# Kernel optimization log

Hardware: AMD Instinct MI355X
Metric: run time of the kernel (lower is better)

## Reference

```python
import jax, jax.numpy as jnp
import numpy as np

D_MODEL = 1024
NUM_HEADS = 16
DEPTH = D_MODEL // NUM_HEADS
B, S = 2, 2048


def setup_inputs() -> dict:
    key = jax.random.key(0)
    ks = jax.random.split(key, 11)
    scale = 1.0 / np.sqrt(D_MODEL)
    inp = {
        "v": jax.random.normal(ks[0], (B, S, D_MODEL), dtype=jnp.float32),
        "k": jax.random.normal(ks[1], (B, S, D_MODEL), dtype=jnp.float32),
        "q": jax.random.normal(ks[2], (B, S, D_MODEL), dtype=jnp.float32),
        "wq": jax.random.normal(ks[3], (D_MODEL, D_MODEL), dtype=jnp.float32) * scale,
        "bq": jnp.zeros((D_MODEL,), dtype=jnp.float32),
        "wk": jax.random.normal(ks[4], (D_MODEL, D_MODEL), dtype=jnp.float32) * scale,
        "bk": jnp.zeros((D_MODEL,), dtype=jnp.float32),
        "wv": jax.random.normal(ks[5], (D_MODEL, D_MODEL), dtype=jnp.float32) * scale,
        "bv": jnp.zeros((D_MODEL,), dtype=jnp.float32),
        "wo": jax.random.normal(ks[6], (D_MODEL, D_MODEL), dtype=jnp.float32) * scale,
        "bo": jnp.zeros((D_MODEL,), dtype=jnp.float32),
    }
    return inp


def _split_heads(x):
    # (B, S, D) -> (B, H, S, depth)
    b, s, _ = x.shape
    return x.reshape(b, s, NUM_HEADS, DEPTH).transpose(0, 2, 1, 3)


def reference(v, k, q, wq, bq, wk, bk, wv, bv, wo, bo):
    qh = _split_heads(q @ wq + bq)  # (B,H,S,d)
    kh = _split_heads(k @ wk + bk)
    vh = _split_heads(v @ wv + bv)
    scores = jnp.einsum("bhqd,bhkd->bhqk", qh, kh) / jnp.sqrt(
        jnp.asarray(DEPTH, dtype=qh.dtype))
    attn = jax.nn.softmax(scores, axis=-1)
    out = jnp.einsum("bhqk,bhkd->bhqd", attn, vh)  # (B,H,S,d)
    out = out.transpose(0, 2, 1, 3).reshape(q.shape[0], -1, D_MODEL)
    return out @ wo + bo
```

## Files before the change

kernel.cpp:

```cpp
#include <hip/hip_runtime.h>
#include <hip/hip_bf16.h>

#define S_LEN 2048
#define DM 1024
#define NH 16
#define DH 64
#define MROWS 4096

typedef __hip_bfloat16 hbf;
typedef __attribute__((ext_vector_type(4))) float floatx4;
typedef __bf16 bf16x8 __attribute__((ext_vector_type(8)));

#define QSCALE 0.18033688f

#define GLOAD_LDS(g, l) __builtin_amdgcn_global_load_lds(                      \
    (const __attribute__((address_space(1))) void*)(g),                        \
    (__attribute__((address_space(3))) void*)(l), 16, 0, 0)


__global__ __launch_bounds__(256) void cvt3w(
    const float* __restrict__ q, const float* __restrict__ k, const float* __restrict__ v,
    hbf* __restrict__ Xqh, hbf* __restrict__ Xkh, hbf* __restrict__ Xvh,
    const float* __restrict__ wq, const float* __restrict__ wk,
    const float* __restrict__ wv, const float* __restrict__ wo,
    hbf* __restrict__ Wqh, hbf* __restrict__ Wkh,
    hbf* __restrict__ Wvh, hbf* __restrict__ Woh) {
  __shared__ float tile[64][65];
  const int t = threadIdx.x;
  if (blockIdx.y < 3) {
    const float* src; hbf* dst;
    switch (blockIdx.y) {
      case 0:  src = q; dst = Xqh; break;
      case 1:  src = k; dst = Xkh; break;
      default: src = v; dst = Xvh; break;
    }
    const int mt = blockIdx.x >> 4, kt = blockIdx.x & 15;
    const int s0 = mt * 64, k0 = kt * 64;
    const int lanep = t & 63, l15p = lanep & 15, quadp = lanep >> 4;
#pragma unroll
    for (int it = 0; it < 2; ++it) {
      int fl = (t >> 6) * 2 + it;
      int fm = fl >> 1, fk = fl & 1;
      const float* rp = &src[(size_t)(s0 + fm * 16 + l15p) * DM + k0 + fk * 32 + quadp * 8];
      const float4 v0 = *(const float4*)rp;
      const float4 v1 = *(const float4*)(rp + 4);
      union { hbf h[8]; uint4 u; } pk;
      pk.h[0] = __float2bfloat16(v0.x); pk.h[1] = __float2bfloat16(v0.y);
      pk.h[2] = __float2bfloat16(v0.z); pk.h[3] = __float2bfloat16(v0.w);
      pk.h[4] = __float2bfloat16(v1.x); pk.h[5] = __float2bfloat16(v1.y);
      pk.h[6] = __float2bfloat16(v1.z); pk.h[7] = __float2bfloat16(v1.w);
      size_t base = ((size_t)(mt * 4 + fm) * 32 + (kt * 2 + fk)) * 512 + lanep * 8;
      *(uint4*)&dst[base] = pk.u;
    }
    return;
  }
  const float* W; hbf* Wh;
  switch (blockIdx.x >> 8) {
    case 0:  W = wq; Wh = Wqh; break;
    case 1:  W = wk; Wh = Wkh; break;
    case 2:  W = wv; Wh = Wvh; break;
    default: W = wo; Wh = Woh; break;
  }
  const int t8 = blockIdx.x & 255;
  const int n0 = (t8 & 15) * 64, k0 = (t8 >> 4) * 64;
  const int c4 = (t & 15) * 4, r16 = t >> 4;
#pragma unroll
  for (int i = 0; i < 4; ++i) {
    int row = i * 16 + r16;
    const float4 vv = *(const float4*)&W[(size_t)(k0 + row) * DM + n0 + c4];
    tile[row][c4 + 0] = vv.x; tile[row][c4 + 1] = vv.y;
    tile[row][c4 + 2] = vv.z; tile[row][c4 + 3] = vv.w;
  }
  __syncthreads();
  {
    const int lane = t & 63, l15w = lane & 15, quadw = lane >> 4, wv_ = t >> 6;
    const int nnl = wv_ * 16 + l15w;
#pragma unroll
    for (int j = 0; j < 2; ++j) {
      const int kk0 = j * 32 + quadw * 8;
      union { hbf h[8]; uint4 u; } pk;
#pragma unroll
      for (int e = 0; e < 8; ++e)
        pk.h[e] = __float2bfloat16(tile[kk0 + e][nnl]);
      size_t base = ((size_t)((n0 + nnl) >> 4) * 32 + ((k0 + kk0) >> 5)) * 512 + lane * 8;
      *(uint4*)&Wh[base] = pk.u;
    }
  }
}

__global__ __launch_bounds__(256) void gemm_qkv(
    const hbf* __restrict__ Xqh, const hbf* __restrict__ Xkh, const hbf* __restrict__ Xvh,
    const hbf* __restrict__ Wqh, const hbf* __restrict__ Wkh, const hbf* __restrict__ Wvh,
    const float* __restrict__ bq, const float* __restrict__ bk, const float* __restrict__ bv,
    hbf* __restrict__ Qh, hbf* __restrict__ Kf, hbf* __restrict__ Vf) {
  const int id = blockIdx.x;
  const int x = id & 7, idx = id >> 3;
  const int z = idx >> 5, rem = idx & 31;
  const int nblk = rem >> 2, mblk = rem & 3;

  const hbf* Ah; const hbf* Bh; const float* bias; hbf* Out; float oscale;
  if (z == 0)      { Ah = Xqh; Bh = Wqh; bias = bq; Out = Qh; oscale = QSCALE; }
  else if (z == 1) { Ah = Xkh; Bh = Wkh; bias = bk; Out = Kf; oscale = 1.0f; }
  else             { Ah = Xvh; Bh = Wvh; bias = bv; Out = Vf; oscale = 1.0f; }

  const int tid = threadIdx.x;
  const int lane = tid & 63, wave = tid >> 6;
  const int wm = wave >> 1, wn = wave & 1;
  const int l15 = lane & 15, quad = lane >> 4;
  const int M0 = x * 512 + mblk * 128 + wm * 64;
  const int n0 = nblk * 128 + wn * 64;

  __shared__ __align__(16) hbf As[2][8][512];
  __shared__ __align__(16) hbf Bs[2][8][512];

  const int sf = (wave & 1) * 4;
  const bool isB = wave >= 2;
  const int mt16 = (x * 512 + mblk * 128) >> 4;
  const int nt16 = (nblk * 128) >> 4;
  const hbf* gbase = isB ? Bh + (size_t)(nt16 + sf) * 32 * 512 + lane * 8
                         : Ah + (size_t)(mt16 + sf) * 32 * 512 + lane * 8;

#pragma unroll
  for (int f = 0; f < 4; ++f) {
    const hbf* g = gbase + (size_t)f * 16384;
    if (isB) GLOAD_LDS(g, &Bs[0][sf + f][0]);
    else     GLOAD_LDS(g, &As[0][sf + f][0]);
  }
  __syncthreads();

  floatx4 acc[4][4] = {};
  int buf = 0;
#pragma unroll 1
  for (int kb = 0; kb < 32; ++kb) {
    if (kb < 31) {
      const int nb = buf ^ 1;
#pragma unroll
      for (int f = 0; f < 4; ++f) {
        const hbf* g = gbase + (size_t)f * 16384 + (size_t)(kb + 1) * 512;
        if (isB) GLOAD_LDS(g, &Bs[nb][sf + f][0]);
        else     GLOAD_LDS(g, &As[nb][sf + f][0]);
      }
    }
    bf16x8 a[4], b[4];
#pragma unroll
    for (int i = 0; i < 4; ++i) {
      a[i] = *(const bf16x8*)&As[buf][wm * 4 + i][lane * 8];
      b[i] = *(const bf16x8*)&Bs[buf][wn * 4 + i][lane * 8];
    }
    __builtin_amdgcn_s_setprio(1);
#pragma unroll
    for (int mi = 0; mi < 4; ++mi)
#pragma unroll
      for (int ni = 0; ni < 4; ++ni)
        acc[mi][ni] = __builtin_amdgcn_mfma_f32_16x16x32_bf16(a[mi], b[ni], acc[mi][ni], 0, 0, 0);
    __builtin_amdgcn_s_setprio(0);
    __syncthreads();
    buf ^= 1;
  }

#pragma unroll
  for (int mi = 0; mi < 4; ++mi) {
#pragma unroll
    for (int ni = 0; ni < 4; ++ni) {
      int col = n0 + ni * 16 + l15;
      float bb_ = bias[col];
#pragma unroll
      for (int r = 0; r < 4; ++r) {
        int row = M0 + mi * 16 + quad * 4 + r;
        float vv = (acc[mi][ni][r] + bb_) * oscale;
        int b = row >> 11, s = row & 2047, h = col >> 6, dd = col & 63;
        int bh = b * NH + h;
        size_t idxo;
        if (z == 1) {
          int kt = s >> 5, nif = (s >> 4) & 1, fl15 = s & 15;
          int ksf = dd >> 5, fquad = (dd >> 3) & 3, e = dd & 7;
          idxo = (((size_t)bh * 64 + kt) * 4 + ksf * 2 + nif) * 512 + (fquad * 16 + fl15) * 8 + e;
        } else if (z == 2) {
          int kt = s >> 5, u = s & 31;
          int p = 2 * (u & 15) + (u >> 4);
          int fquad = p >> 3, e = p & 7;
          int nd = dd >> 4, fl15 = dd & 15;
          idxo = (((size_t)bh * 64 + kt) * 4 + nd) * 512 + (fquad * 16 + fl15) * 8 + e;
        } else {
          idxo = (((size_t)bh * S_LEN + s) << 6) + dd;
        }
        Out[idxo] = __float2bfloat16(vv);
      }
    }
  }
}

__global__ __launch_bounds__(256, 4) void flash_attn(
    const hbf* __restrict__ Qh, const hbf* __restrict__ Kf,
    const hbf* __restrict__ Vf, hbf* __restrict__ AO) {
  const int id = blockIdx.x;
  const int bh = (id & 7) * 4 + (id >> 8);
  const int q0 = ((id >> 3) & 31) * 64;
  const int b = bh >> 4, h = bh & 15;
  const int tid = threadIdx.x;
  const int lane = tid & 63, wave = tid >> 6;
  const int qw = wave & 1;
  const int ksplit = wave >> 1;
  const int l15 = lane & 15, quad = lane >> 4;

  __shared__ __align__(16) unsigned char smem[17408];
  __shared__ float Lbuf[2][32];
  hbf* Pw = (hbf*)(smem + wave * 2560);

  const size_t qbase = (((size_t)bh) * S_LEN + q0 + qw * 32) * DH;
  bf16x8 qf[2][2];
#pragma unroll
  for (int mi = 0; mi < 2; ++mi)
#pragma unroll
    for (int ks = 0; ks < 2; ++ks)
      qf[mi][ks] = *(const bf16x8*)&Qh[qbase + (size_t)(mi * 16 + l15) * DH + ks * 32 + quad * 8];

  bf16x8 ones_f;
  {
    const __bf16 ov = (l15 == 0) ? (__bf16)1.0f : (__bf16)0.0f;
#pragma unroll
    for (int j = 0; j < 8; ++j) ones_f[j] = ov;
  }

  floatx4 o[2][4] = {};
  floatx4 lsum[2] = {};

  const hbf* Kb = Kf + ((size_t)bh * 64 + ksplit * 32) * 2048 + lane * 8;
  const hbf* Vb = Vf + ((size_t)bh * 64 + ksplit * 32) * 2048 + lane * 8;

  bf16x8 kf[2][2], vf[4];
#pragma unroll
  for (int ni = 0; ni < 2; ++ni)
#pragma unroll
    for (int ks = 0; ks < 2; ++ks)
      kf[ni][ks] = *(const bf16x8*)&Kb[(ks * 2 + ni) * 512];
#pragma unroll
  for (int nd = 0; nd < 4; ++nd)
    vf[nd] = *(const bf16x8*)&Vb[nd * 512];

#pragma unroll 1
  for (int it = 0; it < 32; ++it) {
    const int tn = (it + 1) * 2048;

    floatx4 sacc[2][2] = {};
    __builtin_amdgcn_s_setprio(1);
#pragma unroll
    for (int ks = 0; ks < 2; ++ks)
#pragma unroll
      for (int mi = 0; mi < 2; ++mi)
#pragma unroll
        for (int ni = 0; ni < 2; ++ni)
          sacc[mi][ni] = __builtin_amdgcn_mfma_f32_16x16x32_bf16(qf[mi][ks], kf[ni][ks], sacc[mi][ni], 0, 0, 0);
    __builtin_amdgcn_s_setprio(0);

    if (it < 31) {
#pragma unroll
      for (int ni = 0; ni < 2; ++ni)
#pragma unroll
        for (int ks = 0; ks < 2; ++ks)
          kf[ni][ks] = *(const bf16x8*)&Kb[tn + (ks * 2 + ni) * 512];
    }

#pragma unroll
    for (int mi = 0; mi < 2; ++mi)
#pragma unroll
      for (int r = 0; r < 4; ++r) {
        union { hbf h2[2]; unsigned int u; } pk2;
        pk2.h2[0] = __float2bfloat16(__builtin_amdgcn_exp2f(sacc[mi][0][r]));
        pk2.h2[1] = __float2bfloat16(__builtin_amdgcn_exp2f(sacc[mi][1][r]));
        *(unsigned int*)&Pw[(mi * 16 + quad * 4 + r) * 40 + 2 * l15] = pk2.u;
      }

    bf16x8 pf[2];
#pragma unroll
    for (int mi = 0; mi < 2; ++mi)
      pf[mi] = *(const bf16x8*)&Pw[(mi * 16 + l15) * 40 + quad * 8];

    __builtin_amdgcn_s_setprio(1);
#pragma unroll
    for (int mi = 0; mi < 2; ++mi)
      lsum[mi] = __builtin_amdgcn_mfma_f32_16x16x32_bf16(pf[mi], ones_f, lsum[mi], 0, 0, 0);

#pragma unroll
    for (int nd = 0; nd < 4; ++nd)
#pragma unroll
      for (int mi = 0; mi < 2; ++mi)
        o[mi][nd] = __builtin_amdgcn_mfma_f32_16x16x32_bf16(pf[mi], vf[nd], o[mi][nd], 0, 0, 0);
    __builtin_amdgcn_s_setprio(0);

    if (it < 31) {
#pragma unroll
      for (int nd = 0; nd < 4; ++nd)
        vf[nd] = *(const bf16x8*)&Vb[tn + nd * 512];
    }
  }

  __syncthreads();
  if (ksplit == 1) {
    float* Ob = (float*)smem + qw * (32 * 68);
#pragma unroll
    for (int mi = 0; mi < 2; ++mi)
#pragma unroll
      for (int nd = 0; nd < 4; ++nd)
#pragma unroll
        for (int r = 0; r < 4; ++r)
          Ob[(mi * 16 + quad * 4 + r) * 68 + nd * 16 + l15] = o[mi][nd][r];
    if (l15 == 0) {
#pragma unroll
      for (int mi = 0; mi < 2; ++mi)
#pragma unroll
        for (int r = 0; r < 4; ++r)
          Lbuf[qw][mi * 16 + quad * 4 + r] = lsum[mi][r];
    }
  }
  __syncthreads();
  if (ksplit == 0) {
    const float* Ob = (const float*)smem + qw * (32 * 68);
#pragma unroll
    for (int mi = 0; mi < 2; ++mi) {
      float linv[4];
#pragma unroll
      for (int r = 0; r < 4; ++r) {
        float lq = __shfl(lsum[mi][r], lane & 48, 64) + Lbuf[qw][mi * 16 + quad * 4 + r];
        linv[r] = 1.0f / lq;
      }
      const int m16 = (b * S_LEN + q0 + qw * 32 + mi * 16) >> 4;
#pragma unroll
      for (int nd = 0; nd < 4; ++nd) {
        const int kb = h * 2 + (nd >> 1);
        const int qa = ((nd & 1) << 1) + (l15 >> 3);
        const int dd = nd * 16 + l15;
#pragma unroll
        for (int r = 0; r < 4; ++r) {
          int rl = mi * 16 + quad * 4 + r;
          float vv = (o[mi][nd][r] + Ob[rl * 68 + dd]) * linv[r];
          size_t idxo = ((size_t)m16 * 32 + kb) * 512 + (qa * 16 + quad * 4 + r) * 8 + (l15 & 7);
          AO[idxo] = __float2bfloat16(vv);
        }
      }
    }
  }
}

__global__ __launch_bounds__(256) void gemm_out(
    const hbf* __restrict__ Ah, const hbf* __restrict__ Bh,
    const float* __restrict__ bias, float* __restrict__ Out) {
  const int id = blockIdx.x;
  const int x = id & 7, idx = id >> 3;
  const int nblk = idx >> 3, mblk = idx & 7;
  const int tid = threadIdx.x;
  const int lane = tid & 63, wave = tid >> 6;
  const int l15 = lane & 15, quad = lane >> 4;
  const int wm = wave >> 1, wn = wave & 1;
  const int M0 = x * 512 + mblk * 64 + wm * 32;
  const int n0 = nblk * 128 + wn * 64;

  const hbf* ap = Ah + (size_t)(M0 >> 4) * 32 * 512 + lane * 8;
  const hbf* bp = Bh + (size_t)(n0 >> 4) * 32 * 512 + lane * 8;

  floatx4 acc[2][4] = {};
  bf16x8 a0[2], b0[4], a1[2], b1[4];
#pragma unroll
  for (int i = 0; i < 2; ++i) a0[i] = *(const bf16x8*)&ap[(size_t)i * 16384];
#pragma unroll
  for (int i = 0; i < 4; ++i) b0[i] = *(const bf16x8*)&bp[(size_t)i * 16384];

#pragma unroll 1
  for (int kb = 0; kb < 32; kb += 2) {
#pragma unroll
    for (int i = 0; i < 2; ++i) a1[i] = *(const bf16x8*)&ap[(size_t)i * 16384 + (kb + 1) * 512];
#pragma unroll
    for (int i = 0; i < 4; ++i) b1[i] = *(const bf16x8*)&bp[(size_t)i * 16384 + (kb + 1) * 512];
    __builtin_amdgcn_s_setprio(1);
#pragma unroll
    for (int mi = 0; mi < 2; ++mi)
#pragma unroll
      for (int ni = 0; ni < 4; ++ni)
        acc[mi][ni] = __builtin_amdgcn_mfma_f32_16x16x32_bf16(a0[mi], b0[ni], acc[mi][ni], 0, 0, 0);
    __builtin_amdgcn_s_setprio(0);
    const int k2 = kb + 2;
    if (k2 < 32) {
#pragma unroll
      for (int i = 0; i < 2; ++i) a0[i] = *(const bf16x8*)&ap[(size_t)i * 16384 + k2 * 512];
#pragma unroll
      for (int i = 0; i < 4; ++i) b0[i] = *(const bf16x8*)&bp[(size_t)i * 16384 + k2 * 512];
    }
    __builtin_amdgcn_s_setprio(1);
#pragma unroll
    for (int mi = 0; mi < 2; ++mi)
#pragma unroll
      for (int ni = 0; ni < 4; ++ni)
        acc[mi][ni] = __builtin_amdgcn_mfma_f32_16x16x32_bf16(a1[mi], b1[ni], acc[mi][ni], 0, 0, 0);
    __builtin_amdgcn_s_setprio(0);
  }

#pragma unroll
  for (int mi = 0; mi < 2; ++mi) {
#pragma unroll
    for (int ni = 0; ni < 4; ++ni) {
      int col = n0 + ni * 16 + l15;
      float bb_ = bias[col];
#pragma unroll
      for (int r = 0; r < 4; ++r) {
        int row = M0 + mi * 16 + quad * 4 + r;
        Out[(size_t)row * DM + col] = acc[mi][ni][r] + bb_;
      }
    }
  }
}

extern "C" void kernel_launch(void* const* d_in, const int* in_sizes, int n_in,
                              void* d_out, int out_size, void* d_ws, size_t ws_size,
                              hipStream_t stream) {
  const float* v  = (const float*)d_in[0];
  const float* k  = (const float*)d_in[1];
  const float* q  = (const float*)d_in[2];
  const float* wq = (const float*)d_in[3];
  const float* bq = (const float*)d_in[4];
  const float* wk = (const float*)d_in[5];
  const float* bk = (const float*)d_in[6];
  const float* wv = (const float*)d_in[7];
  const float* bv = (const float*)d_in[8];
  const float* wo = (const float*)d_in[9];
  const float* bo = (const float*)d_in[10];

  const size_t NX = (size_t)MROWS * DM;
  const size_t NW = (size_t)DM * DM;
  hbf* base = (hbf*)d_ws;
  hbf* Xqh = base;
  hbf* Xkh = Xqh + NX;
  hbf* Xvh = Xkh + NX;
  hbf* Wqh = Xvh + NX;
  hbf* Wkh = Wqh + NW;
  hbf* Wvh = Wkh + NW;
  hbf* Woh = Wvh + NW;
  hbf* Qh  = Woh + NW;
  hbf* Kf  = Qh + NX;
  hbf* Vf  = Kf + NX;
  hbf* AOh = Vf + NX;

  cvt3w<<<dim3(1024, 4), 256, 0, stream>>>(q, k, v, Xqh, Xkh, Xvh,
                                           wq, wk, wv, wo, Wqh, Wkh, Wvh, Woh);
  gemm_qkv<<<768, 256, 0, stream>>>(Xqh, Xkh, Xvh, Wqh, Wkh, Wvh, bq, bk, bv, Qh, Kf, Vf);
  flash_attn<<<1024, 256, 0, stream>>>(Qh, Kf, Vf, AOh);
  gemm_out<<<512, 256, 0, stream>>>(AOh, Woh, bo, (float*)d_out);
}
```

Measured before the change: 216.9 us.

## Split attention keys four ways per block with 32-query tiles

Each flash-attention block now covers 32 queries instead of 64, and its four waves each take a quarter of the keys instead of two query halves times two key halves. The grid doubles to 2048 blocks, the launch bound asks for 8 blocks per CU, and shared memory shrinks. The per-wave partial outputs are reduced through LDS in two column chunks. This raises parallelism and occupancy, but every block loads K/V for half as many queries, so K/V traffic doubles and the cross-wave reduction gets bigger.

```diff
diff --git a/kernel.cpp b/kernel.cpp
--- a/kernel.cpp
+++ b/kernel.cpp
@@ -190,24 +190,23 @@
   }
 }
 
-__global__ __launch_bounds__(256, 4) void flash_attn(
+__global__ __launch_bounds__(256, 8) void flash_attn(
     const hbf* __restrict__ Qh, const hbf* __restrict__ Kf,
     const hbf* __restrict__ Vf, hbf* __restrict__ AO) {
   const int id = blockIdx.x;
-  const int bh = (id & 7) * 4 + (id >> 8);
-  const int q0 = ((id >> 3) & 31) * 64;
+  const int bh = (id & 7) * 4 + (id >> 9);
+  const int q0 = ((id >> 3) & 63) * 32;
   const int b = bh >> 4, h = bh & 15;
   const int tid = threadIdx.x;
   const int lane = tid & 63, wave = tid >> 6;
-  const int qw = wave & 1;
-  const int ksplit = wave >> 1;
+  const int ksplit = wave;
   const int l15 = lane & 15, quad = lane >> 4;
 
-  __shared__ __align__(16) unsigned char smem[17408];
-  __shared__ float Lbuf[2][32];
+  __shared__ __align__(16) unsigned char smem[13312];
+  __shared__ float Lbuf[3][32];
   hbf* Pw = (hbf*)(smem + wave * 2560);
 
-  const size_t qbase = (((size_t)bh) * S_LEN + q0 + qw * 32) * DH;
+  const size_t qbase = (((size_t)bh) * S_LEN + q0) * DH;
   bf16x8 qf[2][2];
 #pragma unroll
   for (int mi = 0; mi < 2; ++mi)
@@ -225,8 +224,8 @@
   floatx4 o[2][4] = {};
   floatx4 lsum[2] = {};
 
-  const hbf* Kb = Kf + ((size_t)bh * 64 + ksplit * 32) * 2048 + lane * 8;
-  const hbf* Vb = Vf + ((size_t)bh * 64 + ksplit * 32) * 2048 + lane * 8;
+  const hbf* Kb = Kf + ((size_t)bh * 64 + ksplit * 16) * 2048 + lane * 8;
+  const hbf* Vb = Vf + ((size_t)bh * 64 + ksplit * 16) * 2048 + lane * 8;
 
   bf16x8 kf[2][2], vf[4];
 #pragma unroll
@@ -239,7 +238,7 @@
     vf[nd] = *(const bf16x8*)&Vb[nd * 512];
 
 #pragma unroll 1
-  for (int it = 0; it < 32; ++it) {
+  for (int it = 0; it < 16; ++it) {
     const int tn = (it + 1) * 2048;
 
     floatx4 sacc[2][2] = {};
@@ -253,7 +252,7 @@
           sacc[mi][ni] = __builtin_amdgcn_mfma_f32_16x16x32_bf16(qf[mi][ks], kf[ni][ks], sacc[mi][ni], 0, 0, 0);
     __builtin_amdgcn_s_setprio(0);
 
-    if (it < 31) {
+    if (it < 15) {
 #pragma unroll
       for (int ni = 0; ni < 2; ++ni)
 #pragma unroll
@@ -288,52 +287,67 @@
         o[mi][nd] = __builtin_amdgcn_mfma_f32_16x16x32_bf16(pf[mi], vf[nd], o[mi][nd], 0, 0, 0);
     __builtin_amdgcn_s_setprio(0);
 
-    if (it < 31) {
+    if (it < 15) {
 #pragma unroll
       for (int nd = 0; nd < 4; ++nd)
         vf[nd] = *(const bf16x8*)&Vb[tn + nd * 512];
     }
   }
 
-  __syncthreads();
-  if (ksplit == 1) {
-    float* Ob = (float*)smem + qw * (32 * 68);
-#pragma unroll
-    for (int mi = 0; mi < 2; ++mi)
-#pragma unroll
-      for (int nd = 0; nd < 4; ++nd)
-#pragma unroll
-        for (int r = 0; r < 4; ++r)
-          Ob[(mi * 16 + quad * 4 + r) * 68 + nd * 16 + l15] = o[mi][nd][r];
-    if (l15 == 0) {
+  float* Ob = (float*)smem;
+#pragma unroll 1
+  for (int c = 0; c < 2; ++c) {
+    __syncthreads();
+    if (ksplit != 0) {
+      float* Obw = Ob + (ksplit - 1) * (32 * 34);
 #pragma unroll
       for (int mi = 0; mi < 2; ++mi)
 #pragma unroll
-        for (int r = 0; r < 4; ++r)
-          Lbuf[qw][mi * 16 + quad * 4 + r] = lsum[mi][r];
-    }
-  }
-  __syncthreads();
+        for (int j = 0; j < 2; ++j)
+#pragma unroll
+          for (int r = 0; r < 4; ++r)
+            Obw[(mi * 16 + quad * 4 + r) * 34 + j * 16 + l15] = o[mi][c * 2 + j][r];
+      if (c == 0 && l15 == 0) {
+#pragma unroll
+        for (int mi = 0; mi < 2; ++mi)
+#pragma unroll
+          for (int r = 0; r < 4; ++r)
+            Lbuf[ksplit - 1][mi * 16 + quad * 4 + r] = lsum[mi][r];
+      }
+    }
+    __syncthreads();
+    if (ksplit == 0) {
+#pragma unroll
+      for (int mi = 0; mi < 2; ++mi)
+#pragma unroll
+        for (int j = 0; j < 2; ++j)
+#pragma unroll
+          for (int r = 0; r < 4; ++r) {
+            int rl = mi * 16 + quad * 4 + r;
+            o[mi][c * 2 + j][r] += Ob[0 * (32 * 34) + rl * 34 + j * 16 + l15]
+                                 + Ob[1 * (32 * 34) + rl * 34 + j * 16 + l15]
+                                 + Ob[2 * (32 * 34) + rl * 34 + j * 16 + l15];
+          }
+    }
+  }
   if (ksplit == 0) {
-    const float* Ob = (const float*)smem + qw * (32 * 68);
 #pragma unroll
     for (int mi = 0; mi < 2; ++mi) {
       float linv[4];
 #pragma unroll
       for (int r = 0; r < 4; ++r) {
-        float lq = __shfl(lsum[mi][r], lane & 48, 64) + Lbuf[qw][mi * 16 + quad * 4 + r];
+        int rl = mi * 16 + quad * 4 + r;
+        float lq = __shfl(lsum[mi][r], lane & 48, 64) + Lbuf[0][rl] + Lbuf[1][rl] + Lbuf[2][rl];
         linv[r] = 1.0f / lq;
       }
-      const int m16 = (b * S_LEN + q0 + qw * 32 + mi * 16) >> 4;
+      const int m16 = (b * S_LEN + q0 + mi * 16) >> 4;
 #pragma unroll
       for (int nd = 0; nd < 4; ++nd) {
         const int kb = h * 2 + (nd >> 1);
         const int qa = ((nd & 1) << 1) + (l15 >> 3);
-        const int dd = nd * 16 + l15;
 #pragma unroll
         for (int r = 0; r < 4; ++r) {
-          int rl = mi * 16 + quad * 4 + r;
-          float vv = (o[mi][nd][r] + Ob[rl * 68 + dd]) * linv[r];
+          float vv = o[mi][nd][r] * linv[r];
           size_t idxo = ((size_t)m16 * 32 + kb) * 512 + (qa * 16 + quad * 4 + r) * 8 + (l15 & 7);
           AO[idxo] = __float2bfloat16(vv);
         }
@@ -442,6 +456,6 @@
   cvt3w<<<dim3(1024, 4), 256, 0, stream>>>(q, k, v, Xqh, Xkh, Xvh,
                                            wq, wk, wv, wo, Wqh, Wkh, Wvh, Woh);
   gemm_qkv<<<768, 256, 0, stream>>>(Xqh, Xkh, Xvh, Wqh, Wkh, Wvh, bq, bk, bv, Qh, Kf, Vf);
-  flash_attn<<<1024, 256, 0, stream>>>(Qh, Kf, Vf, AOh);
+  flash_attn<<<2048, 256, 0, stream>>>(Qh, Kf, Vf, AOh);
   gemm_out<<<512, 256, 0, stream>>>(AOh, Woh, bo, (float*)d_out);
 }
```

Result: slower. 730.2 us (+236.6%).
